# Optimization experiments

Measured on AMD Instinct MI355X. Metric: run time of the kernel, lower is better.

## Reference

```python
import jax, jax.numpy as jnp
import numpy as np

B, P, E, H = 2, 4096, 512, 8
D = E // H
EPS = 1e-5


def _layernorm2d(x, g, b):
    # LayerNorm over last two dims (patches, embed) jointly, per torch nn.LayerNorm([P, E])
    mu = jnp.mean(x, axis=(-2, -1), keepdims=True)
    var = jnp.mean(jnp.square(x - mu), axis=(-2, -1), keepdims=True)
    return (x - mu) * jax.lax.rsqrt(var + EPS) * g + b


def setup_inputs() -> dict:
    key = jax.random.key(0)
    ks = jax.random.split(key, 4)
    s_in = 1.0 / np.sqrt(E)
    s_hid = 1.0 / np.sqrt(3 * E)
    return {
        "x": jax.random.normal(ks[0], (B, P, E), dtype=jnp.float32),
        "g1": jnp.ones((P, E), jnp.float32),
        "b1": jnp.zeros((P, E), jnp.float32),
        "W1": jax.random.normal(ks[1], (3 * E, E), jnp.float32) * s_in,
        "g2": jnp.ones((P, E), jnp.float32),
        "b2": jnp.zeros((P, E), jnp.float32),
        "Wa": jax.random.normal(ks[2], (3 * E, E), jnp.float32) * s_in,
        "ba": jnp.zeros((3 * E,), jnp.float32),
        "Wb": jax.random.normal(ks[3], (E, 3 * E), jnp.float32) * s_hid,
        "bb": jnp.zeros((E,), jnp.float32),
    }


def reference(x, g1, b1, W1, g2, b2, Wa, ba, Wb, bb):
    # --- attention branch ---
    h = _layernorm2d(x, g1, b1)                      # [B,P,E]
    qkv = h @ W1.T                                   # [B,P,3E]
    qkv = qkv.reshape(B, P, 3, H, D).transpose(2, 0, 3, 1, 4)  # [3,B,H,P,D]
    q, k, v = qkv[0], qkv[1], qkv[2]
    scale = 1.0 / jnp.sqrt(jnp.float32(D))
    dp = jnp.einsum("bhqd,bhkd->bhqk", q, k) * scale  # [B,H,P,P]
    # NOTE: softmax over axis -2 (the query axis), as in the original code
    dp = jax.nn.softmax(dp, axis=-2)
    wv = jnp.einsum("bhqk,bhkd->bhqd", dp, v)        # [B,H,P,D]
    wv = wv.transpose(0, 2, 1, 3).reshape(B, P, E)   # [B,P,E]
    out1 = x + wv
    # --- MLP branch ---
    h2 = _layernorm2d(out1, g2, b2)
    h2 = jax.nn.gelu(h2 @ Wa.T + ba, approximate=False)
    h2 = jax.nn.gelu(h2 @ Wb.T + bb, approximate=False)
    return h2 + out1
```

## Files before the change

kernel.cpp:

```cpp
#include <hip/hip_runtime.h>
#include <math.h>

typedef __bf16 bf16x8 __attribute__((ext_vector_type(8)));
typedef float f32x4 __attribute__((ext_vector_type(4)));
typedef unsigned short u16;
typedef unsigned int u32;

__device__ __forceinline__ void gl_lds16(const void* g, void* l) {
  __builtin_amdgcn_global_load_lds(
      (const __attribute__((address_space(1))) void*)g,
      (__attribute__((address_space(3))) void*)l, 16, 0, 0);
}

__device__ __forceinline__ u16 f2bf(float x) {
  union { float f; u32 u; } v; v.f = x;
  u32 r = v.u + 0x7FFFu + ((v.u >> 16) & 1u);
  return (u16)(r >> 16);
}

__device__ __forceinline__ u32 pack_bf2(float a, float b) {
  union { float f; u32 u; } ua, ub; ua.f = a; ub.f = b;
  return ((ua.u + 0x8000u) >> 16) | ((ub.u + 0x8000u) & 0xFFFF0000u);
}

__device__ __forceinline__ float expfast(float x) {
#if __has_builtin(__builtin_amdgcn_exp2f)
  return __builtin_amdgcn_exp2f(x);
#else
  return exp2f(x);
#endif
}

__device__ __forceinline__ float gelu_f(float v) {
  return 0.5f * v * (1.0f + erff(v * 0.7071067811865475f));
}

__global__ void castbf3(const float* __restrict__ s0, const float* __restrict__ s1,
                        const float* __restrict__ s2, u16* __restrict__ d0,
                        u16* __restrict__ d1, u16* __restrict__ d2) {
  int blk = blockIdx.x;
  const float* s; u16* d;
  if (blk < 768)       { s = s0; d = d0; }
  else if (blk < 1536) { s = s1; d = d1; blk -= 768; }
  else                 { s = s2; d = d2; blk -= 1536; }
  int i = blk * 256 + threadIdx.x;
  float4 v = ((const float4*)s)[i];
  uint2 o;
  o.x = (u32)f2bf(v.x) | ((u32)f2bf(v.y) << 16);
  o.y = (u32)f2bf(v.z) | ((u32)f2bf(v.w) << 16);
  ((uint2*)d)[i] = o;
}

__global__ void ln_reduce(const float* __restrict__ src, float2* __restrict__ part) {
  int b = blockIdx.y;
  const float4* p = (const float4*)(src + (size_t)b * 2097152 + (size_t)blockIdx.x * 16384);
  float s = 0.f, q = 0.f;
  #pragma unroll
  for (int i = 0; i < 16; i++) {
    float4 v = p[i * 256 + threadIdx.x];
    s += v.x + v.y + v.z + v.w;
    q += v.x * v.x + v.y * v.y + v.z * v.z + v.w * v.w;
  }
  #pragma unroll
  for (int off = 32; off; off >>= 1) { s += __shfl_down(s, off, 64); q += __shfl_down(q, off, 64); }
  __shared__ float ls[4], lq[4];
  int w = threadIdx.x >> 6;
  if ((threadIdx.x & 63) == 0) { ls[w] = s; lq[w] = q; }
  __syncthreads();
  if (threadIdx.x == 0)
    part[b * 128 + blockIdx.x] =
        make_float2(ls[0] + ls[1] + ls[2] + ls[3], lq[0] + lq[1] + lq[2] + lq[3]);
}

__global__ void ln_final(const float2* __restrict__ part, float2* __restrict__ stats) {
  int b = blockIdx.x, t = threadIdx.x;
  float2 a = part[b * 128 + t], c = part[b * 128 + 64 + t];
  float s = a.x + c.x, q = a.y + c.y;
  #pragma unroll
  for (int off = 32; off; off >>= 1) { s += __shfl_down(s, off, 64); q += __shfl_down(q, off, 64); }
  if (t == 0) {
    const float inv = 1.0f / 2097152.0f;
    float mu = s * inv, var = q * inv - mu * mu;
    stats[b] = make_float2(mu, rsqrtf(var + 1e-5f));
  }
}

__global__ void ln_apply(const float* __restrict__ src, const float* __restrict__ g,
                         const float* __restrict__ bta, const float2* __restrict__ stats,
                         u16* __restrict__ dst) {
  int i = blockIdx.x * 256 + threadIdx.x;
  int b = i >= 524288;
  float2 st = stats[b];
  int r = i - b * 524288;
  float4 v = ((const float4*)src)[i];
  float4 gv = ((const float4*)g)[r];
  float4 bv = ((const float4*)bta)[r];
  float h0 = (v.x - st.x) * st.y * gv.x + bv.x;
  float h1 = (v.y - st.x) * st.y * gv.y + bv.y;
  float h2 = (v.z - st.x) * st.y * gv.z + bv.z;
  float h3 = (v.w - st.x) * st.y * gv.w + bv.w;
  uint2 o;
  o.x = (u32)f2bf(h0) | ((u32)f2bf(h1) << 16);
  o.y = (u32)f2bf(h2) | ((u32)f2bf(h3) << 16);
  ((uint2*)dst)[i] = o;
}

template <int MODE>
__global__ __launch_bounds__(256, 2)
void gemm_bt(const u16* __restrict__ A, const u16* __restrict__ Bm,
             const float* __restrict__ bias, const float* __restrict__ res,
             float* __restrict__ outf, u16* __restrict__ outb,
             int M, int N, int K) {
  __shared__ u16 As[128 * 32], Bs[128 * 32];
  const int tid = threadIdx.x;
  const int m0 = blockIdx.y * 128, n0 = blockIdx.x * 128;
  const int lane = tid & 63, w = tid >> 6;
  const int wm = (w >> 1) * 64, wn = (w & 1) * 64;
  const int c = lane & 15, quad = lane >> 4;
  const int arow = tid >> 2, acol = (tid & 3) * 8;

  const u16* gA = A + (size_t)(m0 + arow) * K + acol;
  const u16* gB = Bm + (size_t)(n0 + arow) * K + acol;
  u16* lA = As + tid * 8;
  u16* lB = Bs + tid * 8;

  f32x4 acc[4][4] = {};
  for (int kt = 0; kt < K; kt += 32) {
    gl_lds16(gA, lA);
    gl_lds16(gA + (size_t)64 * K, lA + 64 * 32);
    gl_lds16(gB, lB);
    gl_lds16(gB + (size_t)64 * K, lB + 64 * 32);
    gA += 32; gB += 32;
    __syncthreads();
    bf16x8 af[4], bf[4];
    #pragma unroll
    for (int i = 0; i < 4; i++) {
      af[i] = *(const bf16x8*)&As[(wm + i * 16 + c) * 32 + quad * 8];
      bf[i] = *(const bf16x8*)&Bs[(wn + i * 16 + c) * 32 + quad * 8];
    }
    #pragma unroll
    for (int i = 0; i < 4; i++)
      #pragma unroll
      for (int j = 0; j < 4; j++)
        acc[i][j] = __builtin_amdgcn_mfma_f32_16x16x32_bf16(af[i], bf[j], acc[i][j], 0, 0, 0);
    __syncthreads();
  }
  #pragma unroll
  for (int i = 0; i < 4; i++) {
    const int row0 = m0 + wm + i * 16 + quad * 4;
    #pragma unroll
    for (int j = 0; j < 4; j++) {
      const int col = n0 + wn + j * 16 + c;
      #pragma unroll
      for (int r = 0; r < 4; r++) {
        float v = acc[i][j][r];
        size_t oi = (size_t)(row0 + r) * N + col;
        if (MODE == 0 && col < 512) v *= 0.1803368801111204f;
        if (MODE == 1 || MODE == 2) v = gelu_f(v + bias[col]);
        if (MODE == 2) outf[oi] = v + res[oi];
        else           outb[oi] = f2bf(v);
      }
    }
  }
}

__global__ __launch_bounds__(256, 4)
void attn_pass1(const u16* __restrict__ qkv, float* __restrict__ rlpart) {
  __shared__ u16 Qs[2][2 * 128 * 32];
  const int tid = threadIdx.x;
  const int bh = blockIdx.y, b = bh >> 3, h = bh & 7;
  const int k0 = blockIdx.x * 128;
  const int lane = tid & 63, w = tid >> 6;
  const int wn = w * 32;
  const int c = lane & 15, quad = lane >> 4;
  const int arow = tid >> 2, acol = (tid & 3) * 8;

  bf16x8 bk[2][2];
  {
    const u16* Kg = qkv + ((size_t)(b * 4096 + k0 + wn + c)) * 1536 + 512 + h * 64 + quad * 8;
    #pragma unroll
    for (int j = 0; j < 2; j++)
      #pragma unroll
      for (int ks = 0; ks < 2; ks++)
        bk[j][ks] = *(const bf16x8*)(Kg + (size_t)j * 16 * 1536 + ks * 32);
  }
  const u16* Qg = qkv + ((size_t)(b * 4096 + blockIdx.z * 2048)) * 1536 + h * 64;

  #define STAGE_Q(t)                                                              \
    {                                                                             \
      u16* dst = Qs[(t) & 1];                                                     \
      const u16* src = Qg + (size_t)((t) * 128) * 1536;                           \
      _Pragma("unroll")                                                           \
      for (int ks = 0; ks < 2; ks++)                                              \
        _Pragma("unroll")                                                         \
        for (int rr = 0; rr < 128; rr += 64)                                      \
          gl_lds16(src + (size_t)(rr + arow) * 1536 + ks * 32 + acol,             \
                   dst + ks * 4096 + (rr + arow) * 32 + acol);                    \
    }

  STAGE_Q(0);
  float s0 = 0.f, s1 = 0.f;
  for (int t = 0; t < 16; t++) {
    __syncthreads();
    if (t + 1 < 16) STAGE_Q(t + 1);
    const u16* buf = Qs[t & 1];
    #pragma unroll
    for (int i = 0; i < 8; i++) {
      bf16x8 a0 = *(const bf16x8*)&buf[(i * 16 + c) * 32 + quad * 8];
      bf16x8 a1 = *(const bf16x8*)&buf[4096 + (i * 16 + c) * 32 + quad * 8];
      f32x4 acc0 = {}, acc1 = {};
      acc0 = __builtin_amdgcn_mfma_f32_16x16x32_bf16(a0, bk[0][0], acc0, 0, 0, 0);
      acc0 = __builtin_amdgcn_mfma_f32_16x16x32_bf16(a1, bk[0][1], acc0, 0, 0, 0);
      acc1 = __builtin_amdgcn_mfma_f32_16x16x32_bf16(a0, bk[1][0], acc1, 0, 0, 0);
      acc1 = __builtin_amdgcn_mfma_f32_16x16x32_bf16(a1, bk[1][1], acc1, 0, 0, 0);
      #pragma unroll
      for (int r = 0; r < 4; r++) {
        s0 += expfast(acc0[r]);
        s1 += expfast(acc1[r]);
      }
    }
  }
  #undef STAGE_Q
  s0 += __shfl_xor(s0, 16, 64); s0 += __shfl_xor(s0, 32, 64);
  s1 += __shfl_xor(s1, 16, 64); s1 += __shfl_xor(s1, 32, 64);
  if (quad == 0) {
    float* rp = rlpart + ((size_t)blockIdx.z * 16 + bh) * 4096 + k0 + wn;
    rp[c] = s0;
    rp[16 + c] = s1;
  }
}

__global__ void rl_comb(const float* __restrict__ part, float* __restrict__ rl) {
  int i = blockIdx.x * 256 + threadIdx.x;
  rl[i] = 1.0f / (part[i] + part[65536 + i]);
}

__global__ void vtrans(const u16* __restrict__ qkv, const float* __restrict__ rl,
                       u16* __restrict__ vt) {
  __shared__ u16 t[64 * 66];
  int bh = blockIdx.y, p0 = blockIdx.x * 64;
  int b = bh >> 3, h = bh & 7;
  const u16* src = qkv + ((size_t)(b * 4096 + p0)) * 1536 + 1024 + h * 64;
  const float* rp = rl + (size_t)bh * 4096 + p0;
  int tid = threadIdx.x;
  #pragma unroll
  for (int j = 0; j < 16; j++) {
    int idx = j * 256 + tid;
    int p = idx >> 6, d = idx & 63;
    union { float f; u32 u; } uv;
    uv.u = ((u32)src[(size_t)p * 1536 + d]) << 16;
    t[d * 66 + p] = f2bf(uv.f * rp[p]);
  }
  __syncthreads();
  u16* dst = vt + (size_t)bh * 64 * 4096 + p0;
  #pragma unroll
  for (int j = 0; j < 16; j++) {
    int idx = j * 256 + tid;
    int d = idx >> 6, p = idx & 63;
    dst[(size_t)d * 4096 + p] = t[d * 66 + p];
  }
}

__global__ __launch_bounds__(256, 2)
void attn_pass2(const u16* __restrict__ qkv, const u16* __restrict__ vt,
                const float* __restrict__ x, float* __restrict__ out1) {
  __shared__ u16 Ks[2 * 128 * 32];
  __shared__ u16 Vs[4 * 64 * 32];
  __shared__ u16 Ps[4 * 128 * 32];
  const int tid = threadIdx.x;
  const int bh = blockIdx.y, b = bh >> 3, h = bh & 7;
  const int q0 = blockIdx.x * 128;
  const int lane = tid & 63, w = tid >> 6;
  const int wq = w * 32;
  const int c = lane & 15, quad = lane >> 4;
  const int arow = tid >> 2, acol = (tid & 3) * 8;

  bf16x8 bq[2][2];
  {
    const u16* Qg = qkv + ((size_t)(b * 4096 + q0 + wq + c)) * 1536 + h * 64 + quad * 8;
    #pragma unroll
    for (int j = 0; j < 2; j++)
      #pragma unroll
      for (int ks = 0; ks < 2; ks++)
        bq[j][ks] = *(const bf16x8*)(Qg + (size_t)j * 16 * 1536 + ks * 32);
  }
  const u16* Kg = qkv + ((size_t)(b * 4096)) * 1536 + 512 + h * 64;
  const u16* Vg = vt + (size_t)bh * 64 * 4096;

  f32x4 oacc[2][4] = {};
  for (int kt = 0; kt < 32; kt++) {
    const int k0 = kt * 128;
    #pragma unroll
    for (int ks = 0; ks < 2; ks++)
      #pragma unroll
      for (int rr = 0; rr < 128; rr += 64)
        gl_lds16(Kg + (size_t)(k0 + rr + arow) * 1536 + ks * 32 + acol,
                 Ks + ks * 4096 + (rr + arow) * 32 + acol);
    #pragma unroll
    for (int kp = 0; kp < 4; kp++)
      gl_lds16(Vg + (size_t)arow * 4096 + k0 + kp * 32 + acol,
               Vs + kp * 2048 + arow * 32 + acol);
    __syncthreads();

    #pragma unroll
    for (int ih = 0; ih < 2; ih++) {
      f32x4 sacc[4][2] = {};
      #pragma unroll
      for (int i4 = 0; i4 < 4; i4++) {
        const int i = ih * 4 + i4;
        bf16x8 af0 = *(const bf16x8*)&Ks[(i * 16 + c) * 32 + quad * 8];
        bf16x8 af1 = *(const bf16x8*)&Ks[4096 + (i * 16 + c) * 32 + quad * 8];
        sacc[i4][0] = __builtin_amdgcn_mfma_f32_16x16x32_bf16(af0, bq[0][0], sacc[i4][0], 0, 0, 0);
        sacc[i4][0] = __builtin_amdgcn_mfma_f32_16x16x32_bf16(af1, bq[0][1], sacc[i4][0], 0, 0, 0);
        sacc[i4][1] = __builtin_amdgcn_mfma_f32_16x16x32_bf16(af0, bq[1][0], sacc[i4][1], 0, 0, 0);
        sacc[i4][1] = __builtin_amdgcn_mfma_f32_16x16x32_bf16(af1, bq[1][1], sacc[i4][1], 0, 0, 0);
      }
      #pragma unroll
      for (int i4 = 0; i4 < 4; i4++) {
        const int i = ih * 4 + i4;
        #pragma unroll
        for (int j = 0; j < 2; j++) {
          const int qloc = wq + j * 16 + c;
          const int sl = ((i & 1) * 4 + quad) ^ (((qloc >> 1) & 3) << 1);
          u16* pp = Ps + (i >> 1) * 4096 + qloc * 32 + sl * 4;
          float e0 = expfast(sacc[i4][j][0]);
          float e1 = expfast(sacc[i4][j][1]);
          float e2 = expfast(sacc[i4][j][2]);
          float e3 = expfast(sacc[i4][j][3]);
          uint2 pk;
          pk.x = pack_bf2(e0, e1);
          pk.y = pack_bf2(e2, e3);
          *(uint2*)pp = pk;
        }
      }
    }
    #pragma unroll
    for (int ksb = 0; ksb < 4; ksb++) {
      bf16x8 pf[2], vf[4];
      #pragma unroll
      for (int i2 = 0; i2 < 2; i2++) {
        const int qloc = wq + i2 * 16 + c;
        const int blk = quad ^ ((qloc >> 1) & 3);
        pf[i2] = *(const bf16x8*)&Ps[ksb * 4096 + qloc * 32 + blk * 8];
      }
      #pragma unroll
      for (int j2 = 0; j2 < 4; j2++)
        vf[j2] = *(const bf16x8*)&Vs[ksb * 2048 + (j2 * 16 + c) * 32 + quad * 8];
      #pragma unroll
      for (int i2 = 0; i2 < 2; i2++)
        #pragma unroll
        for (int j2 = 0; j2 < 4; j2++)
          oacc[i2][j2] = __builtin_amdgcn_mfma_f32_16x16x32_bf16(pf[i2], vf[j2], oacc[i2][j2], 0, 0, 0);
    }
    __syncthreads();
  }
  #pragma unroll
  for (int i2 = 0; i2 < 2; i2++)
    #pragma unroll
    for (int j2 = 0; j2 < 4; j2++)
      #pragma unroll
      for (int r = 0; r < 4; r++) {
        const int q = q0 + wq + i2 * 16 + quad * 4 + r;
        const int d = j2 * 16 + c;
        size_t oi = ((size_t)(b * 4096 + q)) * 512 + h * 64 + d;
        out1[oi] = x[oi] + oacc[i2][j2][r];
      }
}

extern "C" void kernel_launch(void* const* d_in, const int* in_sizes, int n_in,
                              void* d_out, int out_size, void* d_ws, size_t ws_size,
                              hipStream_t stream) {
  const float* x  = (const float*)d_in[0];
  const float* g1 = (const float*)d_in[1];
  const float* b1 = (const float*)d_in[2];
  const float* W1 = (const float*)d_in[3];
  const float* g2 = (const float*)d_in[4];
  const float* b2 = (const float*)d_in[5];
  const float* Wa = (const float*)d_in[6];
  const float* ba = (const float*)d_in[7];
  const float* Wb = (const float*)d_in[8];
  const float* bb = (const float*)d_in[9];
  float* out = (float*)d_out;

  char* ws = (char*)d_ws;
  u16* w1b   = (u16*)(ws);
  u16* wab   = (u16*)(ws + 1572864);
  u16* wbb   = (u16*)(ws + 3145728);
  u16* h1    = (u16*)(ws + 4718592);
  u16* qkv   = (u16*)(ws + 13107200);
  u16* vt    = (u16*)(ws + 38273024);
  u16* h2    = (u16*)(ws + 46661632);
  u16* mid   = (u16*)(ws + 55050240);
  float* rl  = (float*)(ws + 80216064);
  float* o1  = (float*)(ws + 80478208);
  float2* part  = (float2*)(ws + 97255424);
  float2* stats = (float2*)(ws + 97257472);
  float* rlpart = (float*)(ws + 55050240);

  castbf3<<<2304, 256, 0, stream>>>(W1, Wa, Wb, w1b, wab, wbb);

  ln_reduce<<<dim3(128, 2), 256, 0, stream>>>(x, part);
  ln_final<<<2, 64, 0, stream>>>(part, stats);
  ln_apply<<<4096, 256, 0, stream>>>(x, g1, b1, stats, h1);

  gemm_bt<0><<<dim3(12, 64), 256, 0, stream>>>(h1, w1b, nullptr, nullptr, nullptr, qkv,
                                               8192, 1536, 512);
  attn_pass1<<<dim3(32, 16, 2), 256, 0, stream>>>(qkv, rlpart);
  rl_comb<<<256, 256, 0, stream>>>(rlpart, rl);
  vtrans<<<dim3(64, 16), 256, 0, stream>>>(qkv, rl, vt);
  attn_pass2<<<dim3(32, 16), 256, 0, stream>>>(qkv, vt, x, o1);

  ln_reduce<<<dim3(128, 2), 256, 0, stream>>>(o1, part);
  ln_final<<<2, 64, 0, stream>>>(part, stats);
  ln_apply<<<4096, 256, 0, stream>>>(o1, g2, b2, stats, h2);

  gemm_bt<1><<<dim3(12, 64), 256, 0, stream>>>(h2, wab, ba, nullptr, nullptr, mid,
                                               8192, 1536, 512);
  gemm_bt<2><<<dim3(4, 64), 256, 0, stream>>>(mid, wbb, bb, o1, out, nullptr,
                                              8192, 512, 1536);
}
```

Before: 384.0 us.

## Double-buffer K/V tiles and feed P from registers via 16x16x16 MFMA

The attention pass2 loop now uses 64-key tiles with double-buffered LDS staging, prefetching the next K/V tile while computing the current one, so each iteration needs one barrier instead of two. The exponentiated scores are kept in registers as bf16x4 fragments and fed directly into 16x16x16 MFMAs, which removes the LDS round-trip for P. The V-transpose kernel writes a tiled, XOR-swizzled layout so each 64-key V tile is contiguous and can be read with fewer bank conflicts. The cost is twice as many half-K MFMA instructions for the PV product and more loop iterations.

New measurement: 389.0 us. About the same (+1.3%).

```diff
diff --git a/kernel.cpp b/kernel.cpp
--- a/kernel.cpp
+++ b/kernel.cpp
@@ -2,7 +2,10 @@
 #include <math.h>
 
 typedef __bf16 bf16x8 __attribute__((ext_vector_type(8)));
+typedef __bf16 bf16x4 __attribute__((ext_vector_type(4)));
+typedef short s16x4 __attribute__((ext_vector_type(4)));
 typedef float f32x4 __attribute__((ext_vector_type(4)));
+typedef unsigned int u32x2 __attribute__((ext_vector_type(2)));
 typedef unsigned short u16;
 typedef unsigned int u32;
 
@@ -28,6 +31,15 @@
   return __builtin_amdgcn_exp2f(x);
 #else
   return exp2f(x);
+#endif
+}
+
+__device__ __forceinline__ f32x4 mfma16(bf16x4 a, bf16x4 b, f32x4 c) {
+#if __has_builtin(__builtin_amdgcn_mfma_f32_16x16x16_bf16)
+  return __builtin_amdgcn_mfma_f32_16x16x16_bf16(a, b, c, 0, 0, 0);
+#else
+  return __builtin_amdgcn_mfma_f32_16x16x16bf16_1k(
+      __builtin_bit_cast(s16x4, a), __builtin_bit_cast(s16x4, b), c, 0, 0, 0);
 #endif
 }
 
@@ -252,28 +264,26 @@
     t[d * 66 + p] = f2bf(uv.f * rp[p]);
   }
   __syncthreads();
-  u16* dst = vt + (size_t)bh * 64 * 4096 + p0;
+  u16* dst = vt + (size_t)bh * 262144 + (size_t)blockIdx.x * 4096;
   #pragma unroll
   for (int j = 0; j < 16; j++) {
     int idx = j * 256 + tid;
     int d = idx >> 6, p = idx & 63;
-    dst[(size_t)d * 4096 + p] = t[d * 66 + p];
+    dst[d * 64 + ((((p >> 3) & 7) ^ (d & 7)) << 3) + (p & 7)] = t[d * 66 + p];
   }
 }
 
 __global__ __launch_bounds__(256, 2)
 void attn_pass2(const u16* __restrict__ qkv, const u16* __restrict__ vt,
                 const float* __restrict__ x, float* __restrict__ out1) {
-  __shared__ u16 Ks[2 * 128 * 32];
-  __shared__ u16 Vs[4 * 64 * 32];
-  __shared__ u16 Ps[4 * 128 * 32];
+  __shared__ u16 Ks[2][2][2048];
+  __shared__ u16 Vs[2][4096];
   const int tid = threadIdx.x;
   const int bh = blockIdx.y, b = bh >> 3, h = bh & 7;
   const int q0 = blockIdx.x * 128;
   const int lane = tid & 63, w = tid >> 6;
   const int wq = w * 32;
   const int c = lane & 15, quad = lane >> 4;
-  const int arow = tid >> 2, acol = (tid & 3) * 8;
 
   bf16x8 bq[2][2];
   {
@@ -284,76 +294,62 @@
       for (int ks = 0; ks < 2; ks++)
         bq[j][ks] = *(const bf16x8*)(Qg + (size_t)j * 16 * 1536 + ks * 32);
   }
-  const u16* Kg = qkv + ((size_t)(b * 4096)) * 1536 + 512 + h * 64;
-  const u16* Vg = vt + (size_t)bh * 64 * 4096;
-
+  const u16* Kg = qkv + ((size_t)b * 4096) * 1536 + 512 + h * 64;
+  const u16* Vg = vt + (size_t)bh * 262144;
+
+  #define STAGE_KV(t)                                                             \
+    {                                                                             \
+      const int buf_ = (t) & 1;                                                   \
+      const int krow_ = (t) * 64 + (tid >> 2);                                    \
+      _Pragma("unroll")                                                           \
+      for (int ks = 0; ks < 2; ks++)                                              \
+        gl_lds16(Kg + (size_t)krow_ * 1536 + ks * 32 + (tid & 3) * 8,             \
+                 &Ks[buf_][ks][tid * 8]);                                         \
+      gl_lds16(Vg + (t) * 4096 + tid * 8, &Vs[buf_][tid * 8]);                    \
+      gl_lds16(Vg + (t) * 4096 + 2048 + tid * 8, &Vs[buf_][2048 + tid * 8]);      \
+    }
+
+  STAGE_KV(0);
   f32x4 oacc[2][4] = {};
-  for (int kt = 0; kt < 32; kt++) {
-    const int k0 = kt * 128;
-    #pragma unroll
-    for (int ks = 0; ks < 2; ks++)
-      #pragma unroll
-      for (int rr = 0; rr < 128; rr += 64)
-        gl_lds16(Kg + (size_t)(k0 + rr + arow) * 1536 + ks * 32 + acol,
-                 Ks + ks * 4096 + (rr + arow) * 32 + acol);
-    #pragma unroll
-    for (int kp = 0; kp < 4; kp++)
-      gl_lds16(Vg + (size_t)arow * 4096 + k0 + kp * 32 + acol,
-               Vs + kp * 2048 + arow * 32 + acol);
+  for (int t = 0; t < 64; t++) {
     __syncthreads();
-
-    #pragma unroll
-    for (int ih = 0; ih < 2; ih++) {
-      f32x4 sacc[4][2] = {};
-      #pragma unroll
-      for (int i4 = 0; i4 < 4; i4++) {
-        const int i = ih * 4 + i4;
-        bf16x8 af0 = *(const bf16x8*)&Ks[(i * 16 + c) * 32 + quad * 8];
-        bf16x8 af1 = *(const bf16x8*)&Ks[4096 + (i * 16 + c) * 32 + quad * 8];
-        sacc[i4][0] = __builtin_amdgcn_mfma_f32_16x16x32_bf16(af0, bq[0][0], sacc[i4][0], 0, 0, 0);
-        sacc[i4][0] = __builtin_amdgcn_mfma_f32_16x16x32_bf16(af1, bq[0][1], sacc[i4][0], 0, 0, 0);
-        sacc[i4][1] = __builtin_amdgcn_mfma_f32_16x16x32_bf16(af0, bq[1][0], sacc[i4][1], 0, 0, 0);
-        sacc[i4][1] = __builtin_amdgcn_mfma_f32_16x16x32_bf16(af1, bq[1][1], sacc[i4][1], 0, 0, 0);
-      }
-      #pragma unroll
-      for (int i4 = 0; i4 < 4; i4++) {
-        const int i = ih * 4 + i4;
-        #pragma unroll
-        for (int j = 0; j < 2; j++) {
-          const int qloc = wq + j * 16 + c;
-          const int sl = ((i & 1) * 4 + quad) ^ (((qloc >> 1) & 3) << 1);
-          u16* pp = Ps + (i >> 1) * 4096 + qloc * 32 + sl * 4;
-          float e0 = expfast(sacc[i4][j][0]);
-          float e1 = expfast(sacc[i4][j][1]);
-          float e2 = expfast(sacc[i4][j][2]);
-          float e3 = expfast(sacc[i4][j][3]);
-          uint2 pk;
-          pk.x = pack_bf2(e0, e1);
-          pk.y = pack_bf2(e2, e3);
-          *(uint2*)pp = pk;
-        }
-      }
-    }
-    #pragma unroll
-    for (int ksb = 0; ksb < 4; ksb++) {
-      bf16x8 pf[2], vf[4];
-      #pragma unroll
-      for (int i2 = 0; i2 < 2; i2++) {
-        const int qloc = wq + i2 * 16 + c;
-        const int blk = quad ^ ((qloc >> 1) & 3);
-        pf[i2] = *(const bf16x8*)&Ps[ksb * 4096 + qloc * 32 + blk * 8];
-      }
-      #pragma unroll
-      for (int j2 = 0; j2 < 4; j2++)
-        vf[j2] = *(const bf16x8*)&Vs[ksb * 2048 + (j2 * 16 + c) * 32 + quad * 8];
-      #pragma unroll
-      for (int i2 = 0; i2 < 2; i2++)
-        #pragma unroll
-        for (int j2 = 0; j2 < 4; j2++)
-          oacc[i2][j2] = __builtin_amdgcn_mfma_f32_16x16x32_bf16(pf[i2], vf[j2], oacc[i2][j2], 0, 0, 0);
-    }
-    __syncthreads();
-  }
+    if (t + 1 < 64) STAGE_KV(t + 1);
+    const int buf = t & 1;
+
+    f32x4 sacc[4][2] = {};
+    #pragma unroll
+    for (int i = 0; i < 4; i++) {
+      bf16x8 af0 = *(const bf16x8*)&Ks[buf][0][(i * 16 + c) * 32 + quad * 8];
+      bf16x8 af1 = *(const bf16x8*)&Ks[buf][1][(i * 16 + c) * 32 + quad * 8];
+      #pragma unroll
+      for (int j = 0; j < 2; j++) {
+        sacc[i][j] = __builtin_amdgcn_mfma_f32_16x16x32_bf16(af0, bq[j][0], sacc[i][j], 0, 0, 0);
+        sacc[i][j] = __builtin_amdgcn_mfma_f32_16x16x32_bf16(af1, bq[j][1], sacc[i][j], 0, 0, 0);
+      }
+    }
+    bf16x4 pa[4][2];
+    #pragma unroll
+    for (int i = 0; i < 4; i++)
+      #pragma unroll
+      for (int j = 0; j < 2; j++) {
+        u32x2 pk;
+        pk.x = pack_bf2(expfast(sacc[i][j][0]), expfast(sacc[i][j][1]));
+        pk.y = pack_bf2(expfast(sacc[i][j][2]), expfast(sacc[i][j][3]));
+        pa[i][j] = __builtin_bit_cast(bf16x4, pk);
+      }
+    #pragma unroll
+    for (int kc = 0; kc < 4; kc++) {
+      const int kb = 2 * kc + (quad >> 1);
+      #pragma unroll
+      for (int j2 = 0; j2 < 4; j2++) {
+        const int d = j2 * 16 + c;
+        bf16x4 vf = *(const bf16x4*)&Vs[buf][d * 64 + ((kb ^ (d & 7)) << 3) + 4 * (quad & 1)];
+        oacc[0][j2] = mfma16(pa[kc][0], vf, oacc[0][j2]);
+        oacc[1][j2] = mfma16(pa[kc][1], vf, oacc[1][j2]);
+      }
+    }
+  }
+  #undef STAGE_KV
   #pragma unroll
   for (int i2 = 0; i2 < 2; i2++)
     #pragma unroll
```
